# Performance work log

Hardware: AMD Instinct MI355X
Metric: run time of the kernel (lower is better)

## Reference

```python
import jax, jax.numpy as jnp
import numpy as np
from jax import lax

# 4D convolution via lax.conv_general_dilated (supports N spatial dims natively)
# Layout: x is (N, C, T, U, V, W); weight is (O, I, kT, kU, kV, kW)

def conv4d(x, w, b):
    dn = lax.conv_dimension_numbers(x.shape, w.shape, ('NCTUVW', 'OITUVW', 'NCTUVW'))
    y = lax.conv_general_dilated(x, w, window_strides=(1, 1, 1, 1), padding='SAME',
                                 dimension_numbers=dn)
    return y + b[None, :, None, None, None, None]


def setup_inputs() -> dict:
    key = jax.random.key(0)
    k0, k1, k2, k3, k4 = jax.random.split(key, 5)
    B, C_in, C_hid, C_out = 2, 64, 128, 64
    T, D, H, W = 4, 16, 32, 32
    K = 3  # kernel size per dim (stmode 'C' -> (3,3,3,3))
    x = jax.random.normal(k0, (B, C_in, T, D, H, W), dtype=jnp.float32)
    scale1 = 1.0 / np.sqrt(C_in * K ** 4)
    scale2 = 1.0 / np.sqrt(C_hid * K ** 4)
    w1 = jax.random.normal(k1, (C_hid, C_in, K, K, K, K), dtype=jnp.float32) * scale1
    b1 = jax.random.normal(k2, (C_hid,), dtype=jnp.float32) * scale1
    w2 = jax.random.normal(k3, (C_out, C_hid, K, K, K, K), dtype=jnp.float32) * scale2
    b2 = jax.random.normal(k4, (C_out,), dtype=jnp.float32) * scale2
    return {"x": x, "w1": w1, "b1": b1, "w2": w2, "b2": b2}


def reference(x, w1, b1, w2, b2):
    # conv1 -> ReLU -> (dropout p=0 is identity) -> conv2 -> (dropout identity)
    h = jax.nn.relu(conv4d(x, w1, b1))
    return conv4d(h, w2, b2)
```

## Files before the change

kernel.cpp:

```cpp
#include <hip/hip_runtime.h>


using bf16x8 = __attribute__((ext_vector_type(8))) __bf16;
using f32x16 = __attribute__((ext_vector_type(16))) float;
using f32x4  = __attribute__((ext_vector_type(4))) float;

typedef __attribute__((address_space(1))) const void as1_void;
typedef __attribute__((address_space(3))) void as3_void;
__device__ __forceinline__ void gload_lds16(const void* g, void* l) {
    __builtin_amdgcn_global_load_lds((as1_void*)g, (as3_void*)l, 16, 0, 0);
}

__global__ __launch_bounds__(256) void cvt_x(const float* __restrict__ x,
                                             __bf16* __restrict__ x_t) {
    __shared__ float lt[64][65];
    const int nb = blockIdx.y;
    const int p0 = blockIdx.x * 64;
    const int tu = p0 >> 10;
    const float* src = x + (size_t)nb * 64 * 65536;
    __bf16* dst = x_t + (size_t)nb * 65536 * 64;
    #pragma unroll
    for (int i = 0; i < 16; ++i) {
        int idx = i * 256 + threadIdx.x;
        int c = idx >> 6, p = idx & 63;
        lt[c][p] = src[(size_t)c * 65536 + p0 + p];
    }
    __syncthreads();
    #pragma unroll
    for (int it = 0; it < 2; ++it) {
        int idx = it * 256 + threadIdx.x;
        int pl = idx & 63;
        int chunk = idx >> 6;
        int p = p0 + pl;
        int v = (p >> 5) & 31, w = p & 31;
        bf16x8 pk;
        #pragma unroll
        for (int e = 0; e < 8; ++e)
            pk[e] = (__bf16)lt[chunk * 8 + e][pl];
        *(bf16x8*)(dst + (size_t)(tu * 32 + v) * 2048 + chunk * 256 + w * 8) = pk;
    }
}

template <int CIN>
__global__ __launch_bounds__(256) void cvt_w(const float* __restrict__ w,
                                             __bf16* __restrict__ wt) {
    constexpr int COUT = 8192 / CIN;
    constexpr int LOGC = (CIN == 64) ? 7 : 6;
    const int tap = blockIdx.x;
    __bf16* dst = wt + (size_t)tap * 8192;
    #pragma unroll
    for (int it = 0; it < 32; ++it) {
        const int i  = it * 256 + threadIdx.x;
        const int cl = i & 15;
        const int o  = (i >> 4) & (COUT - 1);
        const int kg = i >> (4 + LOGC);
        dst[i] = (__bf16)w[(size_t)(o * CIN + kg * 16 + cl) * 81 + tap];
    }
}

template <int CIN, int COUT, int GM, int GN, int WPEU, bool RELU>
__global__ __launch_bounds__(256, WPEU) void conv4d_mfma(
    const __bf16* __restrict__ in_t,
    const __bf16* __restrict__ wt,
    const float* __restrict__ bias,
    __bf16* __restrict__ out_bf,
    float* __restrict__ out_f)
{
    constexpr int KST   = CIN / 16;
    constexpr int UNITS = CIN / 32;
    constexpr int LOGU  = (UNITS == 2) ? 1 : 2;
    constexpr int VSPAN = GM * 4;
    constexpr int VGB   = (VSPAN == 4) ? 3 : 2;
    constexpr int ROWS  = VSPAN + 2;
    constexpr int SLOTS = ROWS * 136;
    constexpr int RNDS  = (SLOTS + 255) / 256;
    constexpr int BUFB  = SLOTS * 16;

    __shared__ __bf16 tile[2 * SLOTS * 8];

    const int tid  = threadIdx.x;
    const int lane = tid & 63;
    const int l31  = lane & 31;
    const int hl   = lane >> 5;
    const int wv   = tid >> 6;
    const int gmi  = (GM == 2) ? (wv >> 1) : 0;
    const int gni  = (GM == 2) ? (wv & 1) : wv;

    const int bid = blockIdx.x;
    const int xcd = bid & 7;
    const int s0  = bid >> 3;
    const int u   = xcd * 2 + (s0 & 1);
    const int vg  = (s0 >> 1) & ((1 << VGB) - 1);
    const int t   = (s0 >> (1 + VGB)) & 3;
    const int nb  = (s0 >> (3 + VGB)) & 1;
    const int v0  = vg * VSPAN;
    const int pbase = ((t * 16 + u) * 32 + v0) * 32;

    const __bf16* inb = in_t + (size_t)nb * 65536 * CIN;

    int goff[RNDS];
    #pragma unroll
    for (int r = 0; r < RNDS; ++r) {
        const int slot = r * 256 + tid;
        const int row  = slot / 136;
        const int rem  = slot - row * 136;
        const int chunk = rem / 34;
        const int wp   = rem - chunk * 34;
        const int v_in = v0 - 1 + row;
        const int w_in = wp - 1;
        const bool ok = (slot < SLOTS) && ((unsigned)v_in < 32u) &&
                        ((unsigned)w_in < 32u);
        goff[r] = ok ? (v_in * (CIN * 32) + chunk * 256 + w_in * 8) : -1;
    }

    #pragma unroll
    for (int r = 0; r < RNDS; ++r) {
        const int slot = r * 256 + tid;
        if (slot < SLOTS && goff[r] < 0) {
            *(uint4*)((char*)tile + slot * 16) = make_uint4(0u, 0u, 0u, 0u);
            *(uint4*)((char*)tile + BUFB + slot * 16) = make_uint4(0u, 0u, 0u, 0u);
        }
    }

    const int lane_base = gmi * 4 * 136 + hl * 34 + l31;
    const bf16x8* tile16 = (const bf16x8*)tile;

    const __bf16* wlane = wt + ((size_t)(gni * 32 + l31)) * 16 + hl * 8;

    int sb[9], tb0[9], nst = 0;
    #pragma unroll
    for (int kt = 0; kt < 3; ++kt) {
        const int t_in = t + kt - 1;
        if ((unsigned)t_in >= 4u) continue;
        #pragma unroll
        for (int ku = 0; ku < 3; ++ku) {
            const int u_in = u + ku - 1;
            if ((unsigned)u_in >= 16u) continue;
            sb[nst]  = (t_in * 16 + u_in) * 1024 * CIN;
            tb0[nst] = (kt * 3 + ku) * 9;
            ++nst;
        }
    }
    const int U = nst * UNITS;

    f32x16 acc[4];
    #pragma unroll
    for (int mt = 0; mt < 4; ++mt)
        #pragma unroll
        for (int i = 0; i < 16; ++i)
            acc[mt][i] = 0.f;

    auto issue = [&](int j) {
        const int st = j >> LOGU, ch = j & (UNITS - 1);
        const __bf16* gb = inb + sb[st] + ch * 1024;
        char* lb = ((char*)tile) + (j & 1) * BUFB + wv * 1024;
        #pragma unroll
        for (int r = 0; r < RNDS; ++r)
            if (goff[r] >= 0)
                gload_lds16(gb + goff[r], lb + r * 4096);
    };

    auto ldA = [&](const bf16x8* tb, int ks, int kw, bf16x8 (&af)[6]) {
        #pragma unroll
        for (int j = 0; j < 6; ++j)
            af[j] = tb[j * 136 + ks * 68 + kw];
    };
    auto ldB = [&](int tapb, int ch, int ks, int kw, bf16x8 (&bv)[3]) {
        const int ksg = ch * 2 + ks;
        #pragma unroll
        for (int kv = 0; kv < 3; ++kv) {
            const int wo = ((tapb + kv * 3 + kw) * KST + ksg) * (COUT * 16);
            bv[kv] = *(const bf16x8*)(wlane + wo);
        }
    };
    auto mfma12 = [&](bf16x8 (&af)[6], bf16x8 (&bv)[3]) {
        __builtin_amdgcn_s_setprio(1);
        #pragma unroll
        for (int kv = 0; kv < 3; ++kv)
            #pragma unroll
            for (int rr = 0; rr < 4; ++rr)
                acc[rr] = __builtin_amdgcn_mfma_f32_32x32x16_bf16(
                    af[rr + kv], bv[kv], acc[rr], 0, 0, 0);
        __builtin_amdgcn_s_setprio(0);
    };

    issue(0);
    bf16x8 bvP[3];
    ldB(tb0[0], 0, 0, 0, bvP);

    #pragma unroll 1
    for (int i = 0; i < U; ++i) {
        asm volatile("s_waitcnt vmcnt(0) lgkmcnt(0)" ::: "memory");
        __syncthreads();

        const int st = i >> LOGU, ch = i & (UNITS - 1);
        const int tapb = tb0[st];
        const bf16x8* tb = tile16 + (i & 1) * SLOTS + lane_base;
        const bool more = (i + 1 < U);

        bf16x8 afA[6], afB[6], bvX[3], bvY[3];
        ldA(tb, 0, 0, afA);
        ldA(tb, 0, 1, afB); ldB(tapb, ch, 0, 1, bvX);
        mfma12(afA, bvP);
        ldA(tb, 0, 2, afA); ldB(tapb, ch, 0, 2, bvY);
        mfma12(afB, bvX);
        ldA(tb, 1, 0, afB); ldB(tapb, ch, 1, 0, bvX);
        mfma12(afA, bvY);
        ldA(tb, 1, 1, afA); ldB(tapb, ch, 1, 1, bvY);
        if (more) issue(i + 1);
        mfma12(afB, bvX);
        ldA(tb, 1, 2, afB); ldB(tapb, ch, 1, 2, bvX);
        mfma12(afA, bvY);
        if (more)
            ldB(tb0[(i + 1) >> LOGU], (i + 1) & (UNITS - 1), 0, 0, bvP);
        mfma12(afB, bvX);
    }

    {
        const int o = gni * 32 + l31;
        const float bvls = bias[o];
        #pragma unroll
        for (int rr = 0; rr < 4; ++rr) {
            const int pb = pbase + (gmi * 4 + rr) * 32;
            if constexpr (RELU) {
                #pragma unroll
                for (int rg = 0; rg < 4; ++rg)
                    #pragma unroll
                    for (int j = 0; j < 4; ++j) {
                        float v = acc[rr][rg * 4 + j] + bvls;
                        v = v > 0.f ? v : 0.f;
                        const int p = pb + j + 8 * rg + 4 * hl;
                        const int vv = (p >> 5) & 31, ww = p & 31, tu = p >> 10;
                        out_bf[(size_t)nb * 65536 * COUT +
                               (size_t)(tu * 32 + vv) * (32 * COUT) +
                               (o >> 3) * 256 + ww * 8 + (o & 7)] = (__bf16)v;
                    }
            } else {
                #pragma unroll
                for (int rg = 0; rg < 4; ++rg) {
                    f32x4 sv;
                    #pragma unroll
                    for (int j = 0; j < 4; ++j)
                        sv[j] = acc[rr][rg * 4 + j] + bvls;
                    const int p = pb + 8 * rg + 4 * hl;
                    *(f32x4*)(out_f + ((size_t)nb * COUT + o) * 65536 + p) = sv;
                }
            }
        }
    }
}

extern "C" void kernel_launch(void* const* d_in, const int* in_sizes, int n_in,
                              void* d_out, int out_size, void* d_ws, size_t ws_size,
                              hipStream_t stream) {
    const float* x  = (const float*)d_in[0];
    const float* w1 = (const float*)d_in[1];
    const float* b1 = (const float*)d_in[2];
    const float* w2 = (const float*)d_in[3];
    const float* b2 = (const float*)d_in[4];
    float* out = (float*)d_out;

    char* ws = (char*)d_ws;
    __bf16* x_t = (__bf16*)ws;
    __bf16* h_t = (__bf16*)(ws + 16777216);
    __bf16* w1t = (__bf16*)(ws + 50331648);
    __bf16* w2t = (__bf16*)(ws + 51658752);

    cvt_x<<<dim3(1024, 2), 256, 0, stream>>>(x, x_t);
    cvt_w<64><<<81, 256, 0, stream>>>(w1, w1t);
    cvt_w<128><<<81, 256, 0, stream>>>(w2, w2t);

    conv4d_mfma<64, 128, 1, 4, 2, true><<<1024, 256, 0, stream>>>(x_t, w1t, b1, h_t,
                                                                  nullptr);
    conv4d_mfma<128, 64, 2, 2, 2, false><<<512, 256, 0, stream>>>(h_t, w2t, b2,
                                                                  nullptr, out);
}
```

Measured before the change: 396.5 us.

## Shrink conv blocks to 128 threads and pipeline loads with partial waitcnt

Both conv kernels now run with 128-thread blocks, each covering a 4-row spatial tile and 64 output channels. The first conv splits its output channels across two blocks, so both convs launch more blocks. Padding slots are filled from a zeroed global page instead of being zeroed in LDS, which lets every load round issue unconditionally. The next unit's tile load is issued right after the barrier, a partial vmcnt wait lets it overlap compute, all six weight fragments are double-buffered in registers, and the MFMA priority toggles are removed. In exchange, input tiles are reloaded redundantly across channel splits and register pressure rises.

```diff
diff --git a/kernel.cpp b/kernel.cpp
--- a/kernel.cpp
+++ b/kernel.cpp
@@ -12,8 +12,11 @@
 }
 
 __global__ __launch_bounds__(256) void cvt_x(const float* __restrict__ x,
-                                             __bf16* __restrict__ x_t) {
+                                             __bf16* __restrict__ x_t,
+                                             __bf16* __restrict__ zp) {
     __shared__ float lt[64][65];
+    if (blockIdx.x == 0 && blockIdx.y == 0)
+        *(uint4*)((char*)zp + threadIdx.x * 16) = make_uint4(0u, 0u, 0u, 0u);
     const int nb = blockIdx.y;
     const int p0 = blockIdx.x * 64;
     const int tu = p0 >> 10;
@@ -58,42 +61,40 @@
     }
 }
 
-template <int CIN, int COUT, int GM, int GN, int WPEU, bool RELU>
-__global__ __launch_bounds__(256, WPEU) void conv4d_mfma(
+template <int CIN, int COUT, int NSPLIT, bool RELU>
+__global__ __launch_bounds__(128, 2) void conv4d_mfma(
     const __bf16* __restrict__ in_t,
     const __bf16* __restrict__ wt,
     const float* __restrict__ bias,
     __bf16* __restrict__ out_bf,
-    float* __restrict__ out_f)
+    float* __restrict__ out_f,
+    const __bf16* __restrict__ zpage)
 {
-    constexpr int KST   = CIN / 16;
-    constexpr int UNITS = CIN / 32;
-    constexpr int LOGU  = (UNITS == 2) ? 1 : 2;
-    constexpr int VSPAN = GM * 4;
-    constexpr int VGB   = (VSPAN == 4) ? 3 : 2;
-    constexpr int ROWS  = VSPAN + 2;
-    constexpr int SLOTS = ROWS * 136;
-    constexpr int RNDS  = (SLOTS + 255) / 256;
-    constexpr int BUFB  = SLOTS * 16;
-
-    __shared__ __bf16 tile[2 * SLOTS * 8];
+    constexpr int KST     = CIN / 16;
+    constexpr int UNITS   = CIN / 32;
+    constexpr int LOGU    = (UNITS == 2) ? 1 : 2;
+    constexpr int SLOTS   = 6 * 136;
+    constexpr int SLOTS_P = 896;
+    constexpr int RNDS    = 7;
+    constexpr int BUFB_P  = SLOTS_P * 16;
+
+    __shared__ __bf16 tile[2 * SLOTS_P * 8];
 
     const int tid  = threadIdx.x;
     const int lane = tid & 63;
     const int l31  = lane & 31;
     const int hl   = lane >> 5;
     const int wv   = tid >> 6;
-    const int gmi  = (GM == 2) ? (wv >> 1) : 0;
-    const int gni  = (GM == 2) ? (wv & 1) : wv;
 
     const int bid = blockIdx.x;
     const int xcd = bid & 7;
     const int s0  = bid >> 3;
     const int u   = xcd * 2 + (s0 & 1);
-    const int vg  = (s0 >> 1) & ((1 << VGB) - 1);
-    const int t   = (s0 >> (1 + VGB)) & 3;
-    const int nb  = (s0 >> (3 + VGB)) & 1;
-    const int v0  = vg * VSPAN;
+    const int vg  = (s0 >> 1) & 7;
+    const int t   = (s0 >> 4) & 3;
+    const int nb  = (s0 >> 6) & 1;
+    const int nsp = (s0 >> 7) & (NSPLIT - 1);
+    const int v0  = vg * 4;
     const int pbase = ((t * 16 + u) * 32 + v0) * 32;
 
     const __bf16* inb = in_t + (size_t)nb * 65536 * CIN;
@@ -101,7 +102,7 @@
     int goff[RNDS];
     #pragma unroll
     for (int r = 0; r < RNDS; ++r) {
-        const int slot = r * 256 + tid;
+        const int slot = r * 128 + tid;
         const int row  = slot / 136;
         const int rem  = slot - row * 136;
         const int chunk = rem / 34;
@@ -113,19 +114,11 @@
         goff[r] = ok ? (v_in * (CIN * 32) + chunk * 256 + w_in * 8) : -1;
     }
 
-    #pragma unroll
-    for (int r = 0; r < RNDS; ++r) {
-        const int slot = r * 256 + tid;
-        if (slot < SLOTS && goff[r] < 0) {
-            *(uint4*)((char*)tile + slot * 16) = make_uint4(0u, 0u, 0u, 0u);
-            *(uint4*)((char*)tile + BUFB + slot * 16) = make_uint4(0u, 0u, 0u, 0u);
-        }
-    }
-
-    const int lane_base = gmi * 4 * 136 + hl * 34 + l31;
+    const int lane_base = hl * 34 + l31;
     const bf16x8* tile16 = (const bf16x8*)tile;
 
-    const __bf16* wlane = wt + ((size_t)(gni * 32 + l31)) * 16 + hl * 8;
+    const int o = nsp * 64 + wv * 32 + l31;
+    const __bf16* wlane = wt + (size_t)o * 16 + hl * 8;
 
     int sb[9], tb0[9], nst = 0;
     #pragma unroll
@@ -150,14 +143,15 @@
         for (int i = 0; i < 16; ++i)
             acc[mt][i] = 0.f;
 
-    auto issue = [&](int j) {
+    auto issue = [&](int buf, int j) {
         const int st = j >> LOGU, ch = j & (UNITS - 1);
         const __bf16* gb = inb + sb[st] + ch * 1024;
-        char* lb = ((char*)tile) + (j & 1) * BUFB + wv * 1024;
-        #pragma unroll
-        for (int r = 0; r < RNDS; ++r)
-            if (goff[r] >= 0)
-                gload_lds16(gb + goff[r], lb + r * 4096);
+        char* lb = ((char*)tile) + buf * BUFB_P + wv * 1024;
+        #pragma unroll
+        for (int r = 0; r < RNDS; ++r) {
+            const __bf16* ga = (goff[r] >= 0) ? gb + goff[r] : zpage;
+            gload_lds16(ga, lb + r * 2048);
+        }
     };
 
     auto ldA = [&](const bf16x8* tb, int ks, int kw, bf16x8 (&af)[6]) {
@@ -174,54 +168,55 @@
         }
     };
     auto mfma12 = [&](bf16x8 (&af)[6], bf16x8 (&bv)[3]) {
-        __builtin_amdgcn_s_setprio(1);
         #pragma unroll
         for (int kv = 0; kv < 3; ++kv)
             #pragma unroll
             for (int rr = 0; rr < 4; ++rr)
                 acc[rr] = __builtin_amdgcn_mfma_f32_32x32x16_bf16(
                     af[rr + kv], bv[kv], acc[rr], 0, 0, 0);
-        __builtin_amdgcn_s_setprio(0);
-    };
-
-    issue(0);
-    bf16x8 bvP[3];
-    ldB(tb0[0], 0, 0, 0, bvP);
+    };
+
+    issue(0, 0);
+    bf16x8 bv[6][3];
+    #pragma unroll
+    for (int g = 0; g < 6; ++g)
+        ldB(tb0[0], 0, g / 3, g % 3, bv[g]);
 
     #pragma unroll 1
     for (int i = 0; i < U; ++i) {
-        asm volatile("s_waitcnt vmcnt(0) lgkmcnt(0)" ::: "memory");
-        __syncthreads();
-
-        const int st = i >> LOGU, ch = i & (UNITS - 1);
-        const int tapb = tb0[st];
-        const bf16x8* tb = tile16 + (i & 1) * SLOTS + lane_base;
+        asm volatile("s_waitcnt vmcnt(18)" ::: "memory");
+        __builtin_amdgcn_s_barrier();
+        __builtin_amdgcn_sched_barrier(0);
+
         const bool more = (i + 1 < U);
-
-        bf16x8 afA[6], afB[6], bvX[3], bvY[3];
+        const int nu = more ? i + 1 : i;
+        issue((i + 1) & 1, nu);
+        __builtin_amdgcn_sched_barrier(0);
+
+        const int ntapb = tb0[nu >> LOGU];
+        const int nch   = nu & (UNITS - 1);
+        const bf16x8* tb = tile16 + (i & 1) * SLOTS_P + lane_base;
+
+        bf16x8 afA[6], afB[6];
         ldA(tb, 0, 0, afA);
-        ldA(tb, 0, 1, afB); ldB(tapb, ch, 0, 1, bvX);
-        mfma12(afA, bvP);
-        ldA(tb, 0, 2, afA); ldB(tapb, ch, 0, 2, bvY);
-        mfma12(afB, bvX);
-        ldA(tb, 1, 0, afB); ldB(tapb, ch, 1, 0, bvX);
-        mfma12(afA, bvY);
-        ldA(tb, 1, 1, afA); ldB(tapb, ch, 1, 1, bvY);
-        if (more) issue(i + 1);
-        mfma12(afB, bvX);
-        ldA(tb, 1, 2, afB); ldB(tapb, ch, 1, 2, bvX);
-        mfma12(afA, bvY);
-        if (more)
-            ldB(tb0[(i + 1) >> LOGU], (i + 1) & (UNITS - 1), 0, 0, bvP);
-        mfma12(afB, bvX);
+        ldA(tb, 0, 1, afB);
+        mfma12(afA, bv[0]); ldB(ntapb, nch, 0, 0, bv[0]);
+        ldA(tb, 0, 2, afA);
+        mfma12(afB, bv[1]); ldB(ntapb, nch, 0, 1, bv[1]);
+        ldA(tb, 1, 0, afB);
+        mfma12(afA, bv[2]); ldB(ntapb, nch, 0, 2, bv[2]);
+        ldA(tb, 1, 1, afA);
+        mfma12(afB, bv[3]); ldB(ntapb, nch, 1, 0, bv[3]);
+        ldA(tb, 1, 2, afB);
+        mfma12(afA, bv[4]); ldB(ntapb, nch, 1, 1, bv[4]);
+        mfma12(afB, bv[5]); ldB(ntapb, nch, 1, 2, bv[5]);
     }
 
     {
-        const int o = gni * 32 + l31;
         const float bvls = bias[o];
         #pragma unroll
         for (int rr = 0; rr < 4; ++rr) {
-            const int pb = pbase + (gmi * 4 + rr) * 32;
+            const int pb = pbase + rr * 32;
             if constexpr (RELU) {
                 #pragma unroll
                 for (int rg = 0; rg < 4; ++rg)
@@ -265,13 +260,14 @@
     __bf16* h_t = (__bf16*)(ws + 16777216);
     __bf16* w1t = (__bf16*)(ws + 50331648);
     __bf16* w2t = (__bf16*)(ws + 51658752);
-
-    cvt_x<<<dim3(1024, 2), 256, 0, stream>>>(x, x_t);
+    __bf16* zpg = (__bf16*)(ws + 52985856);
+
+    cvt_x<<<dim3(1024, 2), 256, 0, stream>>>(x, x_t, zpg);
     cvt_w<64><<<81, 256, 0, stream>>>(w1, w1t);
     cvt_w<128><<<81, 256, 0, stream>>>(w2, w2t);
 
-    conv4d_mfma<64, 128, 1, 4, 2, true><<<1024, 256, 0, stream>>>(x_t, w1t, b1, h_t,
-                                                                  nullptr);
-    conv4d_mfma<128, 64, 2, 2, 2, false><<<512, 256, 0, stream>>>(h_t, w2t, b2,
-                                                                  nullptr, out);
-}
+    conv4d_mfma<64, 128, 2, true><<<2048, 128, 0, stream>>>(x_t, w1t, b1, h_t,
+                                                            nullptr, zpg);
+    conv4d_mfma<128, 64, 1, false><<<1024, 128, 0, stream>>>(h_t, w2t, b2,
+                                                             nullptr, out, zpg);
+}
```

Measured after the change: 376.4 us. -5.1%, faster.
